# Kernel tuning notes

Measured on AMD Instinct MI355X. Metric: run time of the kernel, lower is better.

Reference implementation:

```python
import jax, jax.numpy as jnp
import numpy as np

CODEBOOK_DIM = 12          # log2(codebook_size)
CODEBOOK_SIZE = 4096
DIM = 512
INV_TEMPERATURE = 100.0
CODEBOOK_SCALE = 1.0
DIVERSITY_GAMMA = 1.0
ENTROPY_LOSS_WEIGHT = 0.1
EPS = 1e-5


def setup_inputs() -> dict:
    key = jax.random.key(0)
    k_x, k_wi, k_wo = jax.random.split(key, 3)
    x = jax.random.normal(k_x, (4, 4096, DIM), dtype=jnp.float32)
    # nn.Linear weights: (out_features, in_features)
    w_in = jax.random.normal(k_wi, (CODEBOOK_DIM, DIM), dtype=jnp.float32) * 0.02
    b_in = jnp.zeros((CODEBOOK_DIM,), dtype=jnp.float32)
    w_out = jax.random.normal(k_wo, (DIM, CODEBOOK_DIM), dtype=jnp.float32) * 0.02
    b_out = jnp.zeros((DIM,), dtype=jnp.float32)
    return {"x": x, "w_in": w_in, "b_in": b_in, "w_out": w_out, "b_out": b_out}


def _entropy(prob):
    return (-prob * jnp.log(jnp.clip(prob, EPS))).sum(axis=-1)


def _make_codebook():
    mask = (2 ** jnp.arange(CODEBOOK_DIM - 1, -1, -1)).astype(jnp.int32)  # [d]
    all_codes = jnp.arange(CODEBOOK_SIZE, dtype=jnp.int32)
    bits = ((all_codes[:, None] & mask) != 0).astype(jnp.float32)  # [cs, d]
    codebook = bits * CODEBOOK_SCALE * 2 - CODEBOOK_SCALE  # {-1, +1}
    return mask, codebook


def reference(x, w_in, b_in, w_out, b_out):
    mask, codebook = _make_codebook()

    # project in: [b, n, dim] -> [b, n, d]
    xp = jnp.einsum('bnd,cd->bnc', x, w_in) + b_in  # c == codebook_dim here

    # sign quantization (num_codebooks = 1, so c-dim is implicit)
    quantized = jnp.where(xp > 0, CODEBOOK_SCALE, -CODEBOOK_SCALE).astype(xp.dtype)
    indices = ((quantized > 0).astype(jnp.int32) * mask).sum(axis=-1)  # [b, n]

    # straight-through estimator (training path)
    x_st = xp + jax.lax.stop_gradient(quantized - xp)

    # entropy aux loss over full codebook (frac_per_sample_entropy = 1.0)
    flat = xp.reshape(-1, CODEBOOK_DIM)  # original (pre-quant) input, [bn, d]
    # -distance * inv_temp = 2 * inv_temp * <x, code>
    logits = (2.0 * INV_TEMPERATURE) * (flat @ codebook.T)  # [bn, cs]
    prob = jax.nn.softmax(logits, axis=-1)
    per_sample_entropy = _entropy(prob).mean()
    avg_prob = prob.mean(axis=0)  # [cs]
    codebook_entropy = _entropy(avg_prob)
    entropy_aux_loss = per_sample_entropy - DIVERSITY_GAMMA * codebook_entropy
    aux_loss = entropy_aux_loss * ENTROPY_LOSS_WEIGHT

    # project out: [b, n, d] -> [b, n, dim]
    out = jnp.einsum('bnc,dc->bnd', x_st, w_out) + b_out
    return out, indices, aux_loss
```

## Files before the change

### kernel.cpp

```cpp
#include <hip/hip_runtime.h>
#include <hip/hip_bf16.h>


#define NS    16384
#define NOUT  (NS*512)
#define AUXO  (NOUT+NS)
#define INVT2 200.0f
#define NBLK  256

__global__ __launch_bounds__(512, 2) void k_main(
    const float* __restrict__ x,
    const float* __restrict__ w_in,  const float* __restrict__ b_in,
    const float* __restrict__ w_out, const float* __restrict__ b_out,
    float* __restrict__ out, float* __restrict__ idx_out,
    float* __restrict__ P, float* __restrict__ Csum) {

  __shared__ float s_wi[6144];
  __shared__ float s_wt[6144];
  __shared__ float s_phi[64][64];
  __shared__ float s_psi[64][64];
  __shared__ float s_xp[8][8][12];
  __shared__ float s_h[8];

  const int t = threadIdx.x;

  for (int k = 0; k < 12; ++k) {
    int f  = t + k * 512;
    int kk = f & 3;
    int q  = f >> 2;
    int sub = q & 15, e4 = (q >> 4) & 7, d = q >> 7;
    int e  = sub * 32 + e4 * 4 + kk;
    s_wi[f] = w_in[d * 512 + e];
    s_wt[f] = w_out[t * 12 + k];
  }
  __syncthreads();

  const int wave = t >> 6, lane = t & 63;
  const int g = lane >> 4, sub = lane & 15;

  float bin[12];
  #pragma unroll
  for (int d = 0; d < 12; ++d) bin[d] = b_in[d];

  const int i0 = blockIdx.x * 64 + wave * 8 + g;
  const int i1 = i0 + 4;

  const float4* xr0 = (const float4*)(x + (size_t)i0 * 512 + sub * 32);
  const float4* xr1 = (const float4*)(x + (size_t)i1 * 512 + sub * 32);
  float4 xv0[8], xv1[8];
  #pragma unroll
  for (int e4 = 0; e4 < 8; ++e4) { xv0[e4] = xr0[e4]; xv1[e4] = xr1[e4]; }

  float p0[12], p1[12];
  #pragma unroll
  for (int d = 0; d < 12; ++d) { p0[d] = 0.f; p1[d] = 0.f; }
  #pragma unroll
  for (int e4 = 0; e4 < 8; ++e4) {
    #pragma unroll
    for (int d = 0; d < 12; ++d) {
      float4 w4 = ((const float4*)s_wi)[d * 128 + e4 * 16 + sub];
      p0[d] += xv0[e4].x * w4.x + xv0[e4].y * w4.y + xv0[e4].z * w4.z + xv0[e4].w * w4.w;
      p1[d] += xv1[e4].x * w4.x + xv1[e4].y * w4.y + xv1[e4].z * w4.z + xv1[e4].w * w4.w;
    }
  }
  #pragma unroll
  for (int d = 0; d < 12; ++d) {
    #pragma unroll
    for (int m = 1; m <= 8; m <<= 1) {
      p0[d] += __shfl_xor(p0[d], m, 16);
      p1[d] += __shfl_xor(p1[d], m, 16);
    }
    p0[d] += bin[d];
    p1[d] += bin[d];
  }

  unsigned idx0 = 0u, idx1 = 0u;
  #pragma unroll
  for (int d = 0; d < 12; ++d) {
    idx0 |= (p0[d] > 0.f ? 1u : 0u) << (11 - d);
    idx1 |= (p1[d] > 0.f ? 1u : 0u) << (11 - d);
  }
  if (sub == 0) {
    idx_out[i0] = (float)idx0;
    idx_out[i1] = (float)idx1;
    #pragma unroll
    for (int d = 0; d < 12; ++d) {
      s_xp[wave][g][d]     = p0[d];
      s_xp[wave][4 + g][d] = p1[d];
    }
  }

  float sg0[12], sg1[12];
  #pragma unroll
  for (int d = 0; d < 12; ++d) {
    sg0[d] = p0[d] > 0.f ? 1.f : -1.f;
    sg1[d] = p1[d] > 0.f ? 1.f : -1.f;
  }
  float4* or0 = (float4*)(out + (size_t)i0 * 512);
  float4* or1 = (float4*)(out + (size_t)i1 * 512);
  #pragma unroll
  for (int e4 = 0; e4 < 8; ++e4) {
    float4 bo = ((const float4*)b_out)[e4 * 16 + sub];
    float4 o0 = bo, o1 = bo;
    #pragma unroll
    for (int d = 0; d < 12; ++d) {
      float4 w4 = ((const float4*)s_wt)[d * 128 + e4 * 16 + sub];
      o0.x += sg0[d] * w4.x; o0.y += sg0[d] * w4.y; o0.z += sg0[d] * w4.z; o0.w += sg0[d] * w4.w;
      o1.x += sg1[d] * w4.x; o1.y += sg1[d] * w4.y; o1.z += sg1[d] * w4.z; o1.w += sg1[d] * w4.w;
    }
    or0[e4 * 16 + sub] = o0;
    or1[e4 * 16 + sub] = o1;
  }

  float hacc = 0.f;
  #pragma unroll 1
  for (int s = 0; s < 8; ++s) {
    float xq[12];
    #pragma unroll
    for (int d = 0; d < 12; ++d) xq[d] = s_xp[wave][s][d];

    float hi = 0.f, lo = 0.f, ah = 0.f, al = 0.f;
    #pragma unroll
    for (int d = 0; d < 6; ++d) {
      int bh = (lane >> (5 - d)) & 1;
      hi += bh ? xq[d]     : -xq[d];
      lo += bh ? xq[6 + d] : -xq[6 + d];
      ah += fabsf(xq[d]);
      al += fabsf(xq[6 + d]);
    }
    float lhi = INVT2 * (hi - ah);
    float llo = INVT2 * (lo - al);
    float ehi = __expf(lhi);
    float elo = __expf(llo);
    float Shi = ehi, Slo = elo;
    #pragma unroll
    for (int m = 1; m <= 32; m <<= 1) {
      Shi += __shfl_xor(Shi, m);
      Slo += __shfl_xor(Slo, m);
    }
    float phi = ehi / Shi;
    float psi = elo / Slo;
    float lnShi = __logf(Shi), lnSlo = __logf(Slo);
    hacc += phi * (lhi - lnShi) + psi * (llo - lnSlo);

    const int ws = wave * 8 + s;
    s_phi[ws][lane] = phi;
    s_psi[ws][lane] = psi;
  }

  #pragma unroll
  for (int m = 1; m <= 32; m <<= 1) hacc += __shfl_xor(hacc, m);
  if (lane == 0) s_h[wave] = hacc;
  __syncthreads();
  if (t == 0) {
    float hs = 0.f;
    for (int w2 = 0; w2 < 8; ++w2) hs += s_h[w2];
    atomicAdd(Csum, hs);
  }

  const int jb = (t >> 5) * 4;
  const int lb = (t & 31) * 2;
  float a00 = 0.f, a01 = 0.f, a10 = 0.f, a11 = 0.f;
  float a20 = 0.f, a21 = 0.f, a30 = 0.f, a31 = 0.f;
  #pragma unroll 4
  for (int s = 0; s < 64; ++s) {
    float4 ph = *(const float4*)&s_phi[s][jb];
    float2 ps = *(const float2*)&s_psi[s][lb];
    a00 += ph.x * ps.x; a01 += ph.x * ps.y;
    a10 += ph.y * ps.x; a11 += ph.y * ps.y;
    a20 += ph.z * ps.x; a21 += ph.z * ps.y;
    a30 += ph.w * ps.x; a31 += ph.w * ps.y;
  }
  float* Pr = P + (size_t)blockIdx.x * 4096;
  *(float2*)&Pr[(jb + 0) * 64 + lb] = make_float2(a00, a01);
  *(float2*)&Pr[(jb + 1) * 64 + lb] = make_float2(a10, a11);
  *(float2*)&Pr[(jb + 2) * 64 + lb] = make_float2(a20, a21);
  *(float2*)&Pr[(jb + 3) * 64 + lb] = make_float2(a30, a31);
}

__global__ __launch_bounds__(256) void k_reduce(const float* __restrict__ P,
                                                float* __restrict__ Esum) {
  __shared__ float red[16][17];
  __shared__ float ered[16];
  const int t = threadIdx.x;
  const int cl = t & 15, rg = t >> 4;
  const int c = blockIdx.x * 16 + cl;
  float s = 0.f;
  #pragma unroll
  for (int k = 0; k < 16; ++k) s += P[(size_t)(rg + k * 16) * 4096 + c];
  red[rg][cl] = s;
  __syncthreads();
  if (t < 16) {
    float tot = 0.f;
    #pragma unroll
    for (int r = 0; r < 16; ++r) tot += red[r][t];
    float pb = tot * (1.f / (float)NS);
    ered[t] = pb * __logf(fmaxf(pb, 1e-5f));
  }
  __syncthreads();
  if (t == 0) {
    float e = 0.f;
    #pragma unroll
    for (int r = 0; r < 16; ++r) e += ered[r];
    atomicAdd(Esum, e);
  }
}

__global__ void k_final(const float* __restrict__ Csum, const float* __restrict__ Esum,
                        float* __restrict__ aux) {
  if (threadIdx.x == 0) {
    float per_sample_entropy = -Csum[0] * (1.f / (float)NS);
    float codebook_entropy   = -Esum[0];
    aux[0] = 0.1f * (per_sample_entropy - codebook_entropy);
  }
}

extern "C" void kernel_launch(void* const* d_in, const int* in_sizes, int n_in,
                              void* d_out, int out_size, void* d_ws, size_t ws_size,
                              hipStream_t stream) {
  const float* x     = (const float*)d_in[0];
  const float* w_in  = (const float*)d_in[1];
  const float* b_in  = (const float*)d_in[2];
  const float* w_out = (const float*)d_in[3];
  const float* b_out = (const float*)d_in[4];
  float* out = (float*)d_out;

  float* P    = (float*)d_ws;
  float* scal = (float*)((char*)d_ws + (size_t)NBLK * 4096 * 4);

  hipMemsetAsync(scal, 0, 2 * sizeof(float), stream);
  k_main<<<NBLK, 512, 0, stream>>>(x, w_in, b_in, w_out, b_out,
                                   out, out + NOUT, P, scal);
  k_reduce<<<256, 256, 0, stream>>>(P, scal + 1);
  k_final<<<1, 64, 0, stream>>>(scal, scal + 1, out + AUXO);
}
```

Measured before the change: 113.9 us.

## Halve rows per block and double grid to raise occupancy

Each thread now handles one row instead of two, so a block covers 32 samples and the grid doubles to 512 blocks, with launch bounds raised to 4 blocks per CU. This aims to spread work across more CUs and waves and to cut register pressure. In exchange each block reloads both weight matrices into shared memory, twice as many partial-probability tiles go to the workspace, and the reduce kernel reads twice as many partials. Fewer rows per thread also means less memory-level parallelism within a thread.

```diff
diff --git a/kernel.cpp b/kernel.cpp
--- a/kernel.cpp
+++ b/kernel.cpp
@@ -6,9 +6,9 @@
 #define NOUT  (NS*512)
 #define AUXO  (NOUT+NS)
 #define INVT2 200.0f
-#define NBLK  256
-
-__global__ __launch_bounds__(512, 2) void k_main(
+#define NBLK  512
+
+__global__ __launch_bounds__(512, 4) void k_main(
     const float* __restrict__ x,
     const float* __restrict__ w_in,  const float* __restrict__ b_in,
     const float* __restrict__ w_out, const float* __restrict__ b_out,
@@ -17,9 +17,9 @@
 
   __shared__ float s_wi[6144];
   __shared__ float s_wt[6144];
-  __shared__ float s_phi[64][64];
-  __shared__ float s_psi[64][64];
-  __shared__ float s_xp[8][8][12];
+  __shared__ float s_phi[32][64];
+  __shared__ float s_psi[32][64];
+  __shared__ float s_xp[8][4][12];
   __shared__ float s_h[8];
 
   const int t = threadIdx.x;
@@ -42,25 +42,22 @@
   #pragma unroll
   for (int d = 0; d < 12; ++d) bin[d] = b_in[d];
 
-  const int i0 = blockIdx.x * 64 + wave * 8 + g;
-  const int i1 = i0 + 4;
+  const int i0 = blockIdx.x * 32 + wave * 4 + g;
 
   const float4* xr0 = (const float4*)(x + (size_t)i0 * 512 + sub * 32);
-  const float4* xr1 = (const float4*)(x + (size_t)i1 * 512 + sub * 32);
-  float4 xv0[8], xv1[8];
-  #pragma unroll
-  for (int e4 = 0; e4 < 8; ++e4) { xv0[e4] = xr0[e4]; xv1[e4] = xr1[e4]; }
-
-  float p0[12], p1[12];
-  #pragma unroll
-  for (int d = 0; d < 12; ++d) { p0[d] = 0.f; p1[d] = 0.f; }
+  float4 xv0[8];
+  #pragma unroll
+  for (int e4 = 0; e4 < 8; ++e4) xv0[e4] = xr0[e4];
+
+  float p0[12];
+  #pragma unroll
+  for (int d = 0; d < 12; ++d) p0[d] = 0.f;
   #pragma unroll
   for (int e4 = 0; e4 < 8; ++e4) {
     #pragma unroll
     for (int d = 0; d < 12; ++d) {
       float4 w4 = ((const float4*)s_wi)[d * 128 + e4 * 16 + sub];
       p0[d] += xv0[e4].x * w4.x + xv0[e4].y * w4.y + xv0[e4].z * w4.z + xv0[e4].w * w4.w;
-      p1[d] += xv1[e4].x * w4.x + xv1[e4].y * w4.y + xv1[e4].z * w4.z + xv1[e4].w * w4.w;
     }
   }
   #pragma unroll
@@ -68,53 +65,41 @@
     #pragma unroll
     for (int m = 1; m <= 8; m <<= 1) {
       p0[d] += __shfl_xor(p0[d], m, 16);
-      p1[d] += __shfl_xor(p1[d], m, 16);
     }
     p0[d] += bin[d];
-    p1[d] += bin[d];
-  }
-
-  unsigned idx0 = 0u, idx1 = 0u;
+  }
+
+  unsigned idx0 = 0u;
   #pragma unroll
   for (int d = 0; d < 12; ++d) {
     idx0 |= (p0[d] > 0.f ? 1u : 0u) << (11 - d);
-    idx1 |= (p1[d] > 0.f ? 1u : 0u) << (11 - d);
   }
   if (sub == 0) {
     idx_out[i0] = (float)idx0;
-    idx_out[i1] = (float)idx1;
-    #pragma unroll
-    for (int d = 0; d < 12; ++d) {
-      s_xp[wave][g][d]     = p0[d];
-      s_xp[wave][4 + g][d] = p1[d];
-    }
-  }
-
-  float sg0[12], sg1[12];
-  #pragma unroll
-  for (int d = 0; d < 12; ++d) {
-    sg0[d] = p0[d] > 0.f ? 1.f : -1.f;
-    sg1[d] = p1[d] > 0.f ? 1.f : -1.f;
-  }
+    #pragma unroll
+    for (int d = 0; d < 12; ++d) s_xp[wave][g][d] = p0[d];
+  }
+
+  float sg0[12];
+  #pragma unroll
+  for (int d = 0; d < 12; ++d) sg0[d] = p0[d] > 0.f ? 1.f : -1.f;
+
   float4* or0 = (float4*)(out + (size_t)i0 * 512);
-  float4* or1 = (float4*)(out + (size_t)i1 * 512);
   #pragma unroll
   for (int e4 = 0; e4 < 8; ++e4) {
     float4 bo = ((const float4*)b_out)[e4 * 16 + sub];
-    float4 o0 = bo, o1 = bo;
+    float4 o0 = bo;
     #pragma unroll
     for (int d = 0; d < 12; ++d) {
       float4 w4 = ((const float4*)s_wt)[d * 128 + e4 * 16 + sub];
       o0.x += sg0[d] * w4.x; o0.y += sg0[d] * w4.y; o0.z += sg0[d] * w4.z; o0.w += sg0[d] * w4.w;
-      o1.x += sg1[d] * w4.x; o1.y += sg1[d] * w4.y; o1.z += sg1[d] * w4.z; o1.w += sg1[d] * w4.w;
     }
     or0[e4 * 16 + sub] = o0;
-    or1[e4 * 16 + sub] = o1;
   }
 
   float hacc = 0.f;
   #pragma unroll 1
-  for (int s = 0; s < 8; ++s) {
+  for (int s = 0; s < 4; ++s) {
     float xq[12];
     #pragma unroll
     for (int d = 0; d < 12; ++d) xq[d] = s_xp[wave][s][d];
@@ -143,7 +128,7 @@
     float lnShi = __logf(Shi), lnSlo = __logf(Slo);
     hacc += phi * (lhi - lnShi) + psi * (llo - lnSlo);
 
-    const int ws = wave * 8 + s;
+    const int ws = wave * 4 + s;
     s_phi[ws][lane] = phi;
     s_psi[ws][lane] = psi;
   }
@@ -163,7 +148,7 @@
   float a00 = 0.f, a01 = 0.f, a10 = 0.f, a11 = 0.f;
   float a20 = 0.f, a21 = 0.f, a30 = 0.f, a31 = 0.f;
   #pragma unroll 4
-  for (int s = 0; s < 64; ++s) {
+  for (int s = 0; s < 32; ++s) {
     float4 ph = *(const float4*)&s_phi[s][jb];
     float2 ps = *(const float2*)&s_psi[s][lb];
     a00 += ph.x * ps.x; a01 += ph.x * ps.y;
@@ -187,7 +172,7 @@
   const int c = blockIdx.x * 16 + cl;
   float s = 0.f;
   #pragma unroll
-  for (int k = 0; k < 16; ++k) s += P[(size_t)(rg + k * 16) * 4096 + c];
+  for (int k = 0; k < 32; ++k) s += P[(size_t)(rg + k * 16) * 4096 + c];
   red[rg][cl] = s;
   __syncthreads();
   if (t < 16) {
```

Measured after the change: 113.9 us (median of 2 runs). About the same (-0.1%).
